# Kernel tuning notes

Measured on AMD Instinct MI355X. Metric: run time of the kernel, lower is better.

## Reference

```python
import jax, jax.numpy as jnp
import numpy as np

N, F, FH, H = 4096, 512, 64, 8  # nodes, in-features, per-head out-features, heads
ALPHA = 0.2  # LeakyReLU slope


def setup_inputs() -> dict:
    key = jax.random.key(0)
    ks = jax.random.split(key, 6)
    X = jax.random.normal(ks[0], (N, F), dtype=jnp.float32)
    A = (jax.random.uniform(ks[1], (N, N)) < 0.02).astype(jnp.float32)
    glorot_w = (2.0 / (F + FH)) ** 0.5
    glorot_a = (2.0 / (FH + 1)) ** 0.5
    W = jax.random.normal(ks[2], (H, F, FH), dtype=jnp.float32) * glorot_w
    a_self = jax.random.normal(ks[3], (H, FH), dtype=jnp.float32) * glorot_a
    a_neigh = jax.random.normal(ks[4], (H, FH), dtype=jnp.float32) * glorot_a
    b = jnp.zeros((H, FH), dtype=jnp.float32)
    return {"X": X, "A": A, "W": W, "a_self": a_self, "a_neigh": a_neigh, "b": b}


def reference(X, A, W, a_self, a_neigh, b):
    # per-head linear projection: [H, N, FH]
    feats = jnp.einsum('nf,hfo->hno', X, W)
    s_self = jnp.einsum('hno,ho->hn', feats, a_self)    # [H, N]
    s_neigh = jnp.einsum('hno,ho->hn', feats, a_neigh)  # [H, N]
    # additive logits: self_i + neigh_j -> [H, N, N]
    dense = s_self[:, :, None] + s_neigh[:, None, :]
    dense = jnp.where(dense > 0, dense, ALPHA * dense)  # LeakyReLU(0.2)
    dense = dense * A[None, :, :]                       # multiplicative adjacency (as in source)
    attn = jax.nn.softmax(dense, axis=-1)               # full-row softmax (as in source)
    # dropout is identity at inference
    out = jnp.einsum('hij,hjo->hio', attn, feats) + b[:, None, :]  # [H, N, FH]
    out = jnp.transpose(out, (1, 0, 2)).reshape(N, H * FH)         # concat heads
    return jax.nn.relu(out)
```

## Files before the change

kernel.cpp:

```cpp
#include <hip/hip_runtime.h>
#include <hip/hip_bf16.h>

#define N_NODES 4096
#define F_IN 512
#define FHD 64
#define H_HEADS 8
#define C_OUT 512
#define ALPHA 0.2f
#define MAXE 192
#define MAXE_P 200
#define GEMM_BLOCKS 512

typedef __attribute__((ext_vector_type(8))) short bf16x8;
typedef __attribute__((ext_vector_type(4))) float f32x4;

static __device__ __forceinline__ unsigned short f2bf(float f) {
  __hip_bfloat16 h = __float2bfloat16(f);
  union { __hip_bfloat16 h; unsigned short u; } cvt;
  cvt.h = h;
  return cvt.u;
}

__global__ __launch_bounds__(256) void conv_kernel(
    const float* __restrict__ W, unsigned short* __restrict__ WbT,
    float* __restrict__ colsum) {
  __shared__ float sT[64][65];
  const int bid = blockIdx.x;
  const int tid = threadIdx.x;
  if (bid < 64) {
    const int fblk = bid & 7, h = bid >> 3;
#pragma unroll
    for (int i = 0; i < 16; ++i) {
      int idx = tid + i * 256;
      int f = idx >> 6, o = idx & 63;
      sT[f][o] = W[((size_t)h * F_IN + fblk * 64 + f) * FHD + o];
    }
    __syncthreads();
#pragma unroll
    for (int i = 0; i < 16; ++i) {
      int idx = tid + i * 256;
      int o = idx >> 6, f = idx & 63;
      WbT[(size_t)h * FHD * F_IN + (size_t)o * F_IN + fblk * 64 + f] =
          f2bf(sT[f][o]);
    }
  } else {
    colsum[tid] = 0.f;
    colsum[tid + 256] = 0.f;
  }
}

__global__ __launch_bounds__(256) void gemm_scan_kernel(
    const float* __restrict__ X, const unsigned short* __restrict__ WbT,
    const float* __restrict__ a_self, const float* __restrict__ a_neigh,
    const float* __restrict__ A,
    unsigned short* __restrict__ featsb,
    float* __restrict__ s_self, float* __restrict__ s_neigh,
    float* __restrict__ colsum,
    unsigned short* __restrict__ edges, int* __restrict__ degs) {
  __shared__ unsigned short sX[2][64 * 72];
  __shared__ unsigned short sW[2][64 * 72];
  __shared__ float sred[4][64];
  const int bid = blockIdx.x;
  const int tid = threadIdx.x;
  const int wid = tid >> 6, lane = tid & 63;

  if (bid >= GEMM_BLOCKS) {
    const int i = bid - GEMM_BLOCKS;
    int* wave_tot = reinterpret_cast<int*>(&sred[0][0]);
    const float4* __restrict__ Arow4 =
        reinterpret_cast<const float4*>(A + (size_t)i * N_NODES);
    float4 v[4];
#pragma unroll
    for (int q = 0; q < 4; ++q) v[q] = Arow4[tid * 4 + q];
    int mask16 = 0;
#pragma unroll
    for (int q = 0; q < 4; ++q) {
      mask16 |= (v[q].x != 0.f) ? (1 << (q * 4 + 0)) : 0;
      mask16 |= (v[q].y != 0.f) ? (1 << (q * 4 + 1)) : 0;
      mask16 |= (v[q].z != 0.f) ? (1 << (q * 4 + 2)) : 0;
      mask16 |= (v[q].w != 0.f) ? (1 << (q * 4 + 3)) : 0;
    }
    int cnt = __popc(mask16);
    int inc = cnt;
#pragma unroll
    for (int s = 1; s < 64; s <<= 1) {
      int t = __shfl_up(inc, s, 64);
      if (lane >= s) inc += t;
    }
    if (lane == 63) wave_tot[wid] = inc;
    __syncthreads();
    int wprefix = 0, tot = 0;
#pragma unroll
    for (int w = 0; w < 4; ++w) {
      int t = wave_tot[w];
      if (w < wid) wprefix += t;
      tot += t;
    }
    int pos = wprefix + inc - cnt;
    const int jbase = tid * 16;
    unsigned short* __restrict__ erow = edges + (size_t)i * MAXE;
    while (mask16) {
      int k = __ffs(mask16) - 1;
      mask16 &= mask16 - 1;
      if (pos < MAXE) erow[pos] = (unsigned short)(jbase + k);
      ++pos;
    }
    if (tid == 0) degs[i] = tot < MAXE ? tot : MAXE;
    return;
  }

  const int h = bid >> 6;
  const int n0 = (bid & 63) * 64;
  const int l15 = lane & 15, l4 = lane >> 4;

  const int row = tid >> 2, seg = (tid & 3) * 16;
  const float* xsrc = X + (size_t)(n0 + row) * F_IN + seg;
  const unsigned short* wsrc = WbT + ((size_t)h * FHD + row) * F_IN + seg;
  const int soff = row * 72 + seg;

  f32x4 acc[4];
#pragma unroll
  for (int j = 0; j < 4; ++j) acc[j] = (f32x4){0.f, 0.f, 0.f, 0.f};

  {
    float4 xa = *(const float4*)(xsrc);
    float4 xb = *(const float4*)(xsrc + 4);
    float4 xc = *(const float4*)(xsrc + 8);
    float4 xd = *(const float4*)(xsrc + 12);
    bf16x8 p0, p1;
    p0[0] = f2bf(xa.x); p0[1] = f2bf(xa.y); p0[2] = f2bf(xa.z); p0[3] = f2bf(xa.w);
    p0[4] = f2bf(xb.x); p0[5] = f2bf(xb.y); p0[6] = f2bf(xb.z); p0[7] = f2bf(xb.w);
    p1[0] = f2bf(xc.x); p1[1] = f2bf(xc.y); p1[2] = f2bf(xc.z); p1[3] = f2bf(xc.w);
    p1[4] = f2bf(xd.x); p1[5] = f2bf(xd.y); p1[6] = f2bf(xd.z); p1[7] = f2bf(xd.w);
    *(bf16x8*)&sX[0][soff] = p0;
    *(bf16x8*)&sX[0][soff + 8] = p1;
    *(bf16x8*)&sW[0][soff] = *(const bf16x8*)(wsrc);
    *(bf16x8*)&sW[0][soff + 8] = *(const bf16x8*)(wsrc + 8);
  }
  __syncthreads();

  int cur = 0;
  for (int s = 0; s < 8; ++s) {
    float4 xa, xb, xc, xd;
    bf16x8 pw0, pw1;
    const bool pf = (s < 7);
    if (pf) {
      const int k = (s + 1) * 64;
      xa = *(const float4*)(xsrc + k);
      xb = *(const float4*)(xsrc + k + 4);
      xc = *(const float4*)(xsrc + k + 8);
      xd = *(const float4*)(xsrc + k + 12);
      pw0 = *(const bf16x8*)(wsrc + k);
      pw1 = *(const bf16x8*)(wsrc + k + 8);
    }
#pragma unroll
    for (int kk = 0; kk < 2; ++kk) {
      bf16x8 a = *(const bf16x8*)&sX[cur][(wid * 16 + l15) * 72 + kk * 32 + l4 * 8];
#pragma unroll
      for (int tn = 0; tn < 4; ++tn) {
        bf16x8 b = *(const bf16x8*)&sW[cur][(tn * 16 + l15) * 72 + kk * 32 + l4 * 8];
        acc[tn] =
            __builtin_amdgcn_mfma_f32_16x16x32_bf16(a, b, acc[tn], 0, 0, 0);
      }
    }
    if (pf) {
      bf16x8 p0, p1;
      p0[0] = f2bf(xa.x); p0[1] = f2bf(xa.y); p0[2] = f2bf(xa.z); p0[3] = f2bf(xa.w);
      p0[4] = f2bf(xb.x); p0[5] = f2bf(xb.y); p0[6] = f2bf(xb.z); p0[7] = f2bf(xb.w);
      p1[0] = f2bf(xc.x); p1[1] = f2bf(xc.y); p1[2] = f2bf(xc.z); p1[3] = f2bf(xc.w);
      p1[4] = f2bf(xd.x); p1[5] = f2bf(xd.y); p1[6] = f2bf(xd.z); p1[7] = f2bf(xd.w);
      *(bf16x8*)&sX[cur ^ 1][soff] = p0;
      *(bf16x8*)&sX[cur ^ 1][soff + 8] = p1;
      *(bf16x8*)&sW[cur ^ 1][soff] = pw0;
      *(bf16x8*)&sW[cur ^ 1][soff + 8] = pw1;
      __syncthreads();
      cur ^= 1;
    }
  }

  float aS[4], aN[4];
#pragma unroll
  for (int tn = 0; tn < 4; ++tn) {
    aS[tn] = a_self[h * FHD + tn * 16 + l15];
    aN[tn] = a_neigh[h * FHD + tn * 16 + l15];
  }
#pragma unroll
  for (int r = 0; r < 4; ++r) {
    const int grow = n0 + wid * 16 + l4 * 4 + r;
#pragma unroll
    for (int tn = 0; tn < 4; ++tn)
      featsb[(size_t)grow * C_OUT + h * FHD + tn * 16 + l15] =
          f2bf(acc[tn][r]);
    float ps = 0.f, pn = 0.f;
#pragma unroll
    for (int tn = 0; tn < 4; ++tn) {
      float v = acc[tn][r];
      ps = fmaf(v, aS[tn], ps);
      pn = fmaf(v, aN[tn], pn);
    }
#pragma unroll
    for (int sh = 1; sh < 16; sh <<= 1) {
      ps += __shfl_xor(ps, sh, 64);
      pn += __shfl_xor(pn, sh, 64);
    }
    if (l15 == 0) {
      s_self[grow * 8 + h] = ps;
      s_neigh[grow * 8 + h] = pn;
    }
  }

  float psum[4];
#pragma unroll
  for (int tn = 0; tn < 4; ++tn) {
    float s = acc[tn][0] + acc[tn][1] + acc[tn][2] + acc[tn][3];
    s += __shfl_xor(s, 16, 64);
    s += __shfl_xor(s, 32, 64);
    psum[tn] = s;
  }
  __syncthreads();
  if (l4 == 0) {
#pragma unroll
    for (int tn = 0; tn < 4; ++tn) sred[wid][tn * 16 + l15] = psum[tn];
  }
  __syncthreads();
  if (tid < 64) {
    float s = sred[0][tid] + sred[1][tid] + sred[2][tid] + sred[3][tid];
    atomicAdd(&colsum[h * FHD + tid], s);
  }
}

__global__ __launch_bounds__(256) void attn_kernel(
    const unsigned short* __restrict__ edges, const int* __restrict__ degs,
    const unsigned short* __restrict__ featsb,
    const float* __restrict__ s_self, const float* __restrict__ s_neigh,
    const float* __restrict__ colsum, const float* __restrict__ bias,
    float* __restrict__ out) {
  const int i = blockIdx.x;
  const int tid = threadIdx.x;
  const int wid = tid >> 6, lane = tid & 63;
  __shared__ int s_idx[MAXE];
  __shared__ int s_off[MAXE];
  __shared__ float s_w[H_HEADS][MAXE_P];
  __shared__ float sh_self[8];
  __shared__ float sh_e0[8], sh_invZ[8];
  __shared__ float s_part[3][64][9];

  const int deg = degs[i];
  if (tid < 8) sh_self[tid] = s_self[i * 8 + tid];
  if (tid < deg) {
    int j = edges[(size_t)i * MAXE + tid];
    s_idx[tid] = j;
    s_off[tid] = j << 10;
  }
  __syncthreads();

  for (int k = tid; k < deg * 8; k += 256) {
    int e = k >> 3, h = k & 7;
    int j = s_idx[e];
    float l = sh_self[h] + s_neigh[j * 8 + h];
    s_w[h][e] = l > 0.f ? l : ALPHA * l;
  }
  __syncthreads();

#pragma unroll
  for (int p = 0; p < 2; ++p) {
    const int h = wid * 2 + p;
    float m = -1e30f;
    for (int e = lane; e < deg; e += 64) m = fmaxf(m, s_w[h][e]);
#pragma unroll
    for (int s = 32; s > 0; s >>= 1) m = fmaxf(m, __shfl_xor(m, s, 64));
    m = fmaxf(m, 0.0f);
    float e0 = __expf(-m);
    float zs = 0.f;
    for (int e = lane; e < deg; e += 64) {
      float w = __expf(s_w[h][e] - m);
      s_w[h][e] = w - e0;
      zs += w;
    }
#pragma unroll
    for (int s = 32; s > 0; s >>= 1) zs += __shfl_xor(zs, s, 64);
    if (lane == 0) {
      sh_e0[h] = e0;
      sh_invZ[h] = 1.0f / (zs + (float)(N_NODES - deg) * e0);
    }
  }
  __syncthreads();

  const int co = lane;
  const int q = wid;
  const int h = co >> 3;
  const int dq = (deg + 3) >> 2;
  const int ebeg = q * dq;
  const int eend = (ebeg + dq) < deg ? (ebeg + dq) : deg;
  const char* __restrict__ fbase =
      reinterpret_cast<const char*>(featsb) + co * 16;
  float a0 = 0.f, a1 = 0.f, a2 = 0.f, a3 = 0.f;
  float a4 = 0.f, a5 = 0.f, a6 = 0.f, a7 = 0.f;
  float c0 = 0.f, c1 = 0.f, c2 = 0.f, c3 = 0.f;
  float c4 = 0.f, c5 = 0.f, c6 = 0.f, c7 = 0.f;

#define DOT2(accv, pair, wp) \
  asm("v_dot2_f32_bf16 %0, %1, %2, %0" : "+v"(accv) : "v"(pair), "v"(wp))

  int e = ebeg;
  for (; e + 3 < eend; e += 4) {
    float w0 = s_w[h][e], w1 = s_w[h][e + 1];
    float w2 = s_w[h][e + 2], w3 = s_w[h][e + 3];
    unsigned wp01, wp23;
    asm("v_cvt_pk_bf16_f32 %0, %1, %2" : "=v"(wp01) : "v"(w0), "v"(w1));
    asm("v_cvt_pk_bf16_f32 %0, %1, %2" : "=v"(wp23) : "v"(w2), "v"(w3));
    int o0 = s_off[e], o1 = s_off[e + 1];
    int o2 = s_off[e + 2], o3 = s_off[e + 3];
    uint4 u0 = *reinterpret_cast<const uint4*>(fbase + o0);
    uint4 u1 = *reinterpret_cast<const uint4*>(fbase + o1);
    uint4 u2 = *reinterpret_cast<const uint4*>(fbase + o2);
    uint4 u3 = *reinterpret_cast<const uint4*>(fbase + o3);
    unsigned plo, phi;
    plo = __builtin_amdgcn_perm(u1.x, u0.x, 0x05040100u);
    phi = __builtin_amdgcn_perm(u1.x, u0.x, 0x07060302u);
    DOT2(a0, plo, wp01); DOT2(a1, phi, wp01);
    plo = __builtin_amdgcn_perm(u1.y, u0.y, 0x05040100u);
    phi = __builtin_amdgcn_perm(u1.y, u0.y, 0x07060302u);
    DOT2(a2, plo, wp01); DOT2(a3, phi, wp01);
    plo = __builtin_amdgcn_perm(u1.z, u0.z, 0x05040100u);
    phi = __builtin_amdgcn_perm(u1.z, u0.z, 0x07060302u);
    DOT2(a4, plo, wp01); DOT2(a5, phi, wp01);
    plo = __builtin_amdgcn_perm(u1.w, u0.w, 0x05040100u);
    phi = __builtin_amdgcn_perm(u1.w, u0.w, 0x07060302u);
    DOT2(a6, plo, wp01); DOT2(a7, phi, wp01);
    plo = __builtin_amdgcn_perm(u3.x, u2.x, 0x05040100u);
    phi = __builtin_amdgcn_perm(u3.x, u2.x, 0x07060302u);
    DOT2(c0, plo, wp23); DOT2(c1, phi, wp23);
    plo = __builtin_amdgcn_perm(u3.y, u2.y, 0x05040100u);
    phi = __builtin_amdgcn_perm(u3.y, u2.y, 0x07060302u);
    DOT2(c2, plo, wp23); DOT2(c3, phi, wp23);
    plo = __builtin_amdgcn_perm(u3.z, u2.z, 0x05040100u);
    phi = __builtin_amdgcn_perm(u3.z, u2.z, 0x07060302u);
    DOT2(c4, plo, wp23); DOT2(c5, phi, wp23);
    plo = __builtin_amdgcn_perm(u3.w, u2.w, 0x05040100u);
    phi = __builtin_amdgcn_perm(u3.w, u2.w, 0x07060302u);
    DOT2(c6, plo, wp23); DOT2(c7, phi, wp23);
  }
  for (; e < eend; ++e) {
    float w0 = s_w[h][e];
    uint4 u0 = *reinterpret_cast<const uint4*>(fbase + s_off[e]);
    a0 = fmaf(w0, __uint_as_float(u0.x << 16), a0);
    a1 = fmaf(w0, __uint_as_float(u0.x & 0xFFFF0000u), a1);
    a2 = fmaf(w0, __uint_as_float(u0.y << 16), a2);
    a3 = fmaf(w0, __uint_as_float(u0.y & 0xFFFF0000u), a3);
    a4 = fmaf(w0, __uint_as_float(u0.z << 16), a4);
    a5 = fmaf(w0, __uint_as_float(u0.z & 0xFFFF0000u), a5);
    a6 = fmaf(w0, __uint_as_float(u0.w << 16), a6);
    a7 = fmaf(w0, __uint_as_float(u0.w & 0xFFFF0000u), a7);
  }
#undef DOT2
  a0 += c0; a1 += c1; a2 += c2; a3 += c3;
  a4 += c4; a5 += c5; a6 += c6; a7 += c7;

  if (q > 0) {
    float* p = &s_part[q - 1][co][0];
    p[0] = a0; p[1] = a1; p[2] = a2; p[3] = a3;
    p[4] = a4; p[5] = a5; p[6] = a6; p[7] = a7;
  }
  __syncthreads();
  if (q == 0) {
#pragma unroll
    for (int pp = 0; pp < 3; ++pp) {
      const float* p = &s_part[pp][co][0];
      a0 += p[0]; a1 += p[1]; a2 += p[2]; a3 += p[3];
      a4 += p[4]; a5 += p[5]; a6 += p[6]; a7 += p[7];
    }
    const float e0 = sh_e0[h], invZ = sh_invZ[h];
    const float4 cs0 = *reinterpret_cast<const float4*>(&colsum[co * 8]);
    const float4 cs1 = *reinterpret_cast<const float4*>(&colsum[co * 8 + 4]);
    const float4 bb0 = *reinterpret_cast<const float4*>(&bias[co * 8]);
    const float4 bb1 = *reinterpret_cast<const float4*>(&bias[co * 8 + 4]);
    f32x4 o0, o1;
    float v;
    v = (a0 + e0 * cs0.x) * invZ + bb0.x; o0.x = v > 0.f ? v : 0.f;
    v = (a1 + e0 * cs0.y) * invZ + bb0.y; o0.y = v > 0.f ? v : 0.f;
    v = (a2 + e0 * cs0.z) * invZ + bb0.z; o0.z = v > 0.f ? v : 0.f;
    v = (a3 + e0 * cs0.w) * invZ + bb0.w; o0.w = v > 0.f ? v : 0.f;
    v = (a4 + e0 * cs1.x) * invZ + bb1.x; o1.x = v > 0.f ? v : 0.f;
    v = (a5 + e0 * cs1.y) * invZ + bb1.y; o1.y = v > 0.f ? v : 0.f;
    v = (a6 + e0 * cs1.z) * invZ + bb1.z; o1.z = v > 0.f ? v : 0.f;
    v = (a7 + e0 * cs1.w) * invZ + bb1.w; o1.w = v > 0.f ? v : 0.f;
    f32x4* dst = reinterpret_cast<f32x4*>(&out[(size_t)i * C_OUT + co * 8]);
    __builtin_nontemporal_store(o0, dst);
    __builtin_nontemporal_store(o1, dst + 1);
  }
}

extern "C" void kernel_launch(void* const* d_in, const int* in_sizes, int n_in,
                              void* d_out, int out_size, void* d_ws, size_t ws_size,
                              hipStream_t stream) {
  const float* X = (const float*)d_in[0];
  const float* A = (const float*)d_in[1];
  const float* W = (const float*)d_in[2];
  const float* a_self = (const float*)d_in[3];
  const float* a_neigh = (const float*)d_in[4];
  const float* b = (const float*)d_in[5];
  float* out = (float*)d_out;

  char* ws = (char*)d_ws;
  unsigned short* featsb = (unsigned short*)ws;
  char* p = ws + (size_t)N_NODES * C_OUT * 2;
  float* s_self = (float*)p;  p += N_NODES * H_HEADS * 4;
  float* s_neigh = (float*)p; p += N_NODES * H_HEADS * 4;
  float* colsum = (float*)p;  p += C_OUT * 4;
  int* degs = (int*)p;        p += N_NODES * 4;
  unsigned short* edges = (unsigned short*)p;
  p += (size_t)N_NODES * MAXE * 2;
  unsigned short* WbT = (unsigned short*)p;

  conv_kernel<<<65, 256, 0, stream>>>(W, WbT, colsum);
  gemm_scan_kernel<<<GEMM_BLOCKS + N_NODES, 256, 0, stream>>>(
      X, WbT, a_self, a_neigh, A, featsb, s_self, s_neigh, colsum, edges,
      degs);
  attn_kernel<<<N_NODES, 256, 0, stream>>>(edges, degs, featsb, s_self,
                                           s_neigh, colsum, b, out);
}
```

Baseline: 50.70 us.

## Reorder scan blocks first, fuse logit compute into softmax, memset colsum

Puts the adjacency-scan blocks at the front of the fused gemm/scan grid so the row scans dispatch before the GEMM tiles. In the attention kernel, the separate LeakyReLU logit pass and its barrier are removed: each wave computes logits for its two heads directly into registers (up to three edges per lane) before the max/exp reductions. The colsum zeroing moves from the conversion kernel to hipMemsetAsync. This adds a memset launch and hard-codes the MAXE=192 bound as three per-lane slots.

```diff
diff --git a/kernel.cpp b/kernel.cpp
--- a/kernel.cpp
+++ b/kernel.cpp
@@ -22,30 +22,24 @@
 }
 
 __global__ __launch_bounds__(256) void conv_kernel(
-    const float* __restrict__ W, unsigned short* __restrict__ WbT,
-    float* __restrict__ colsum) {
+    const float* __restrict__ W, unsigned short* __restrict__ WbT) {
   __shared__ float sT[64][65];
   const int bid = blockIdx.x;
   const int tid = threadIdx.x;
-  if (bid < 64) {
-    const int fblk = bid & 7, h = bid >> 3;
-#pragma unroll
-    for (int i = 0; i < 16; ++i) {
-      int idx = tid + i * 256;
-      int f = idx >> 6, o = idx & 63;
-      sT[f][o] = W[((size_t)h * F_IN + fblk * 64 + f) * FHD + o];
-    }
-    __syncthreads();
-#pragma unroll
-    for (int i = 0; i < 16; ++i) {
-      int idx = tid + i * 256;
-      int o = idx >> 6, f = idx & 63;
-      WbT[(size_t)h * FHD * F_IN + (size_t)o * F_IN + fblk * 64 + f] =
-          f2bf(sT[f][o]);
-    }
-  } else {
-    colsum[tid] = 0.f;
-    colsum[tid + 256] = 0.f;
+  const int fblk = bid & 7, h = bid >> 3;
+#pragma unroll
+  for (int i = 0; i < 16; ++i) {
+    int idx = tid + i * 256;
+    int f = idx >> 6, o = idx & 63;
+    sT[f][o] = W[((size_t)h * F_IN + fblk * 64 + f) * FHD + o];
+  }
+  __syncthreads();
+#pragma unroll
+  for (int i = 0; i < 16; ++i) {
+    int idx = tid + i * 256;
+    int o = idx >> 6, f = idx & 63;
+    WbT[(size_t)h * FHD * F_IN + (size_t)o * F_IN + fblk * 64 + f] =
+        f2bf(sT[f][o]);
   }
 }
 
@@ -64,8 +58,8 @@
   const int tid = threadIdx.x;
   const int wid = tid >> 6, lane = tid & 63;
 
-  if (bid >= GEMM_BLOCKS) {
-    const int i = bid - GEMM_BLOCKS;
+  if (bid < N_NODES) {
+    const int i = bid;
     int* wave_tot = reinterpret_cast<int*>(&sred[0][0]);
     const float4* __restrict__ Arow4 =
         reinterpret_cast<const float4*>(A + (size_t)i * N_NODES);
@@ -109,8 +103,9 @@
     return;
   }
 
-  const int h = bid >> 6;
-  const int n0 = (bid & 63) * 64;
+  const int g = bid - N_NODES;
+  const int h = g >> 6;
+  const int n0 = (g & 63) * 64;
   const int l15 = lane & 15, l4 = lane >> 4;
 
   const int row = tid >> 2, seg = (tid & 3) * 16;
@@ -254,27 +249,43 @@
   }
   __syncthreads();
 
-  for (int k = tid; k < deg * 8; k += 256) {
-    int e = k >> 3, h = k & 7;
-    int j = s_idx[e];
-    float l = sh_self[h] + s_neigh[j * 8 + h];
-    s_w[h][e] = l > 0.f ? l : ALPHA * l;
-  }
-  __syncthreads();
-
+  const int e0i = lane, e1i = lane + 64, e2i = lane + 128;
 #pragma unroll
   for (int p = 0; p < 2; ++p) {
     const int h = wid * 2 + p;
-    float m = -1e30f;
-    for (int e = lane; e < deg; e += 64) m = fmaxf(m, s_w[h][e]);
+    const float selfh = sh_self[h];
+    float v0 = -1e30f, v1 = -1e30f, v2 = -1e30f;
+    if (e0i < deg) {
+      float l = selfh + s_neigh[s_idx[e0i] * 8 + h];
+      v0 = l > 0.f ? l : ALPHA * l;
+    }
+    if (e1i < deg) {
+      float l = selfh + s_neigh[s_idx[e1i] * 8 + h];
+      v1 = l > 0.f ? l : ALPHA * l;
+    }
+    if (e2i < deg) {
+      float l = selfh + s_neigh[s_idx[e2i] * 8 + h];
+      v2 = l > 0.f ? l : ALPHA * l;
+    }
+    float m = fmaxf(fmaxf(v0, v1), v2);
 #pragma unroll
     for (int s = 32; s > 0; s >>= 1) m = fmaxf(m, __shfl_xor(m, s, 64));
     m = fmaxf(m, 0.0f);
     float e0 = __expf(-m);
     float zs = 0.f;
-    for (int e = lane; e < deg; e += 64) {
-      float w = __expf(s_w[h][e] - m);
-      s_w[h][e] = w - e0;
+    if (e0i < deg) {
+      float w = __expf(v0 - m);
+      s_w[h][e0i] = w - e0;
+      zs += w;
+    }
+    if (e1i < deg) {
+      float w = __expf(v1 - m);
+      s_w[h][e1i] = w - e0;
+      zs += w;
+    }
+    if (e2i < deg) {
+      float w = __expf(v2 - m);
+      s_w[h][e2i] = w - e0;
       zs += w;
     }
 #pragma unroll
@@ -413,8 +424,9 @@
   p += (size_t)N_NODES * MAXE * 2;
   unsigned short* WbT = (unsigned short*)p;
 
-  conv_kernel<<<65, 256, 0, stream>>>(W, WbT, colsum);
-  gemm_scan_kernel<<<GEMM_BLOCKS + N_NODES, 256, 0, stream>>>(
+  hipMemsetAsync(colsum, 0, C_OUT * 4, stream);
+  conv_kernel<<<64, 256, 0, stream>>>(W, WbT);
+  gemm_scan_kernel<<<N_NODES + GEMM_BLOCKS, 256, 0, stream>>>(
       X, WbT, a_self, a_neigh, A, featsb, s_self, s_neigh, colsum, edges,
       degs);
   attn_kernel<<<N_NODES, 256, 0, stream>>>(edges, degs, featsb, s_self,
```

Result: slower. 58.64 us (+15.7%).
